# Performance work log

Measured on AMD Instinct MI355X. Metric: run time of the kernel, lower is better.

Reference implementation:

```python
import jax, jax.numpy as jnp
import numpy as np

N_LUT_IN = 4  # fan-in of every LUT node (the 'n' init arg)
KSIZE = 3


def _lut_level(x, w):
    """x: [O, N, L*n] in [0,1]; w: [O, L, 2^n] LUT tables -> [O, N, L].
    Differentiable LUT = multilinear interpolation over the 2^n corners."""
    O, L = w.shape[0], w.shape[1]
    xi = x.reshape(x.shape[0], x.shape[1], L, N_LUT_IN)
    # iterative doubling builds corner probs without a [.., 2^n, n] broadcast
    p = jnp.ones(xi.shape[:3] + (1,), xi.dtype)
    for i in range(N_LUT_IN):
        xii = xi[..., i:i + 1]
        p = jnp.concatenate([p * (1.0 - xii), p * xii], axis=-1)  # [O,N,L,2^i+1]
    return jnp.einsum('onlc,olc->onl', p, w)


def _lut_tree(flat, ws):
    """flat: [O, N, n_leaf_inputs]; ws: list of per-level LUT tables [O, L_lvl, 16]."""
    x = jax.nn.sigmoid(flat)  # squash real activations into [0,1] for interpolation
    for li, w in enumerate(ws):
        need = w.shape[1] * N_LUT_IN
        pad = need - x.shape[-1]
        if pad > 0:  # pad with 0.5 == sigmoid(0), matching zero-padding of raw inputs
            x = jnp.pad(x, ((0, 0), (0, 0), (0, pad)), constant_values=0.5)
        x = _lut_level(x, w)
        if li < len(ws) - 1:
            x = jax.nn.sigmoid(x)
    return x[..., 0]  # [O, N]


def setup_inputs() -> dict:
    key = jax.random.key(0)
    ks = jax.random.split(key, 5)
    B, C, H, W = 8, 64, 32, 32
    O, Q = 32, 8
    x = jax.random.normal(ks[0], (B, C, H, W), jnp.float32)
    rng = np.random.default_rng(0)
    ci = jnp.asarray(np.stack([rng.permutation(C)[:Q] for _ in range(O)]), jnp.int32)
    # tree level widths for 72 leaf inputs, fan-in 4: 72 -> 18 -> 5 -> 2 -> 1
    w0 = jax.random.normal(ks[1], (O, 18, 16), jnp.float32) * 0.5
    w1 = jax.random.normal(ks[2], (O, 5, 16), jnp.float32) * 0.5
    w2 = jax.random.normal(ks[3], (O, 2, 16), jnp.float32) * 0.5
    w3 = jax.random.normal(ks[4], (O, 1, 16), jnp.float32) * 0.5
    return {'x': x, 'w0': w0, 'w1': w1, 'w2': w2, 'w3': w3, 'channel_indices': ci}


def reference(x, w0, w1, w2, w3, channel_indices):
    B, C, H, W = x.shape
    K = KSIZE
    # unfold: pad=1, stride=1 -> [B, C*K*K, Ho, Wo], feature dim is channel-major (C, K, K)
    patches = jax.lax.conv_general_dilated_patches(
        x, (K, K), (1, 1), ((1, 1), (1, 1)))
    Ho, Wo = patches.shape[2], patches.shape[3]
    patches = patches.reshape(B, C, K, K, Ho, Wo)
    O, Q = channel_indices.shape
    sel = patches[:, channel_indices]  # per-out-channel gather: [B, O, Q, K, K, Ho, Wo]
    # match torch permute(0,2,3,1,4,5): leaf order per pixel is (channel, kh, kw)
    flat = sel.transpose(1, 0, 5, 6, 2, 3, 4).reshape(O, B * Ho * Wo, Q * K * K)
    out = _lut_tree(flat, [w0, w1, w2, w3])  # [O, B*Ho*Wo]
    return out.reshape(O, B, Ho, Wo).transpose(1, 0, 2, 3)  # [B, O, Ho, Wo]
```

## Files before the change

kernel.cpp:

```cpp
#include <hip/hip_runtime.h>

typedef float v2f __attribute__((ext_vector_type(2)));

#define HW 32
#define QD 8

__device__ __forceinline__ float sigmoidf(float v) {
    return __builtin_amdgcn_rcpf(1.0f + __expf(-v));
}

__device__ __forceinline__ v2f sig2(v2f v) {
    v2f r; r.x = sigmoidf(v.x); r.y = sigmoidf(v.y); return r;
}

__device__ __forceinline__ v2f lut4v(const v2f* s, const float* __restrict__ W) {
    v2f a[8];
#pragma unroll
    for (int j = 0; j < 8; ++j) {
        const float d = W[j + 8] - W[j];
        const v2f dv = {d, d}, wv = {W[j], W[j]};
        a[j] = __builtin_elementwise_fma(s[3], dv, wv);
    }
#pragma unroll
    for (int j = 0; j < 4; ++j) a[j] = __builtin_elementwise_fma(s[2], a[j + 4] - a[j], a[j]);
#pragma unroll
    for (int j = 0; j < 2; ++j) a[j] = __builtin_elementwise_fma(s[1], a[j + 2] - a[j], a[j]);
    return __builtin_elementwise_fma(s[0], a[1] - a[0], a[0]);
}

__global__ __launch_bounds__(512, 4) void lt_conv_kernel(
    const float* __restrict__ x,
    const float* __restrict__ w0,
    const float* __restrict__ w1,
    const float* __restrict__ w2,
    const float* __restrict__ w3,
    const int*   __restrict__ ci,
    float*       __restrict__ out)
{
    const int o = blockIdx.x & 31;
    const int b = blockIdx.x >> 5;
    const int tid = threadIdx.x;

    __shared__ float stile[QD * 34 * 34];
    __shared__ int   ldsci[QD];

    if (tid < QD) ldsci[tid] = ci[o * QD + tid];
    __syncthreads();

#pragma unroll
    for (int it = 0; it < 19; ++it) {
        const int idx = tid + it * 512;
        if (idx < QD * 34 * 34) {
            const int q   = idx / 1156;
            const int rem = idx - q * 1156;
            const int row = rem / 34;
            const int col = rem - row * 34;
            const int y = row - 1, xx = col - 1;
            float v = 0.0f;
            if ((unsigned)y < 32u && (unsigned)xx < 32u) {
                const int c = ldsci[q];
                v = x[(((size_t)b * 64 + c) * HW + y) * HW + xx];
            }
            stile[idx] = sigmoidf(v);
        }
    }
    __syncthreads();

    const int wo = tid & 31;
    const int r0 = (tid >> 5) * 2;

    const float* W0 = w0 + o * 18 * 16;
    v2f t[18];
#pragma unroll
    for (int l = 0; l < 18; ++l) {
        v2f p[4];
#pragma unroll
        for (int j = 0; j < 4; ++j) {
            const int flat = 4 * l + j;
            const int q = flat / 9, k = flat - 9 * q;
            const int dy = k / 3, dx = k - 3 * dy;
            const float* base = stile + q * 1156 + (r0 + dy) * 34 + (wo + dx);
            p[j].x = base[0];
            p[j].y = base[34];
        }
        t[l] = sig2(lut4v(p, W0 + l * 16));
    }

    const float* W1 = w1 + o * 5 * 16;
    const v2f h = {0.5f, 0.5f};
    v2f u[5];
#pragma unroll
    for (int l = 0; l < 4; ++l) u[l] = sig2(lut4v(t + 4 * l, W1 + l * 16));
    {
        v2f p[4] = {t[16], t[17], h, h};
        u[4] = sig2(lut4v(p, W1 + 4 * 16));
    }

    const float* W2 = w2 + o * 2 * 16;
    const v2f vv0 = sig2(lut4v(u, W2));
    v2f p1[4] = {u[4], h, h, h};
    const v2f vv1 = sig2(lut4v(p1, W2 + 16));

    const float* W3 = w3 + o * 16;
    v2f p2[4] = {vv0, vv1, h, h};
    const v2f res = lut4v(p2, W3);

    float* op = out + (((size_t)b * 32 + o) * HW + r0) * HW + wo;
    op[0]  = res.x;
    op[HW] = res.y;
}

extern "C" void kernel_launch(void* const* d_in, const int* in_sizes, int n_in,
                              void* d_out, int out_size, void* d_ws, size_t ws_size,
                              hipStream_t stream) {
    const float* x  = (const float*)d_in[0];
    const float* w0 = (const float*)d_in[1];
    const float* w1 = (const float*)d_in[2];
    const float* w2 = (const float*)d_in[3];
    const float* w3 = (const float*)d_in[4];
    const int*   ci = (const int*)d_in[5];
    float* out = (float*)d_out;

    lt_conv_kernel<<<dim3(32 * 8), dim3(512), 0, stream>>>(x, w0, w1, w2, w3, ci, out);
}
```

Before: 80.15 us.

## Split image into half-height blocks and pack two LUTs per v2f lane

Launches twice as many blocks, each covering 16 output rows with an 18-row halo tile. Each thread now computes one pixel, and the packed-float math pairs two different LUT nodes of the same level instead of two pixels. The odd nodes that do not pair up use a new scalar path. The aim is more parallelism across the GPU's CUs and lower per-thread register pressure, at the cost of extra halo loads and extra sigmoid work when filling the tile.

```diff
diff --git a/kernel.cpp b/kernel.cpp
--- a/kernel.cpp
+++ b/kernel.cpp
@@ -4,6 +4,9 @@
 
 #define HW 32
 #define QD 8
+#define ROWS 18
+#define TW 34
+#define TILE (ROWS * TW)
 
 __device__ __forceinline__ float sigmoidf(float v) {
     return __builtin_amdgcn_rcpf(1.0f + __expf(-v));
@@ -13,12 +16,13 @@
     v2f r; r.x = sigmoidf(v.x); r.y = sigmoidf(v.y); return r;
 }
 
-__device__ __forceinline__ v2f lut4v(const v2f* s, const float* __restrict__ W) {
+__device__ __forceinline__ v2f lut4p(const v2f* s, const float* __restrict__ Wa,
+                                     const float* __restrict__ Wb) {
     v2f a[8];
 #pragma unroll
     for (int j = 0; j < 8; ++j) {
-        const float d = W[j + 8] - W[j];
-        const v2f dv = {d, d}, wv = {W[j], W[j]};
+        const v2f dv = {Wa[j + 8] - Wa[j], Wb[j + 8] - Wb[j]};
+        const v2f wv = {Wa[j], Wb[j]};
         a[j] = __builtin_elementwise_fma(s[3], dv, wv);
     }
 #pragma unroll
@@ -27,6 +31,19 @@
     for (int j = 0; j < 2; ++j) a[j] = __builtin_elementwise_fma(s[1], a[j + 2] - a[j], a[j]);
     return __builtin_elementwise_fma(s[0], a[1] - a[0], a[0]);
 }
+
+__device__ __forceinline__ float lut4s(const float* s, const float* __restrict__ W) {
+    float a[8];
+#pragma unroll
+    for (int j = 0; j < 8; ++j) a[j] = fmaf(s[3], W[j + 8] - W[j], W[j]);
+#pragma unroll
+    for (int j = 0; j < 4; ++j) a[j] = fmaf(s[2], a[j + 4] - a[j], a[j]);
+#pragma unroll
+    for (int j = 0; j < 2; ++j) a[j] = fmaf(s[1], a[j + 2] - a[j], a[j]);
+    return fmaf(s[0], a[1] - a[0], a[0]);
+}
+
+#define TGET(k) (((k) & 1) ? t2[(k) >> 1].y : t2[(k) >> 1].x)
 
 __global__ __launch_bounds__(512, 4) void lt_conv_kernel(
     const float* __restrict__ x,
@@ -37,25 +54,28 @@
     const int*   __restrict__ ci,
     float*       __restrict__ out)
 {
-    const int o = blockIdx.x & 31;
-    const int b = blockIdx.x >> 5;
-    const int tid = threadIdx.x;
+    const int bi = blockIdx.x;
+    const int o = bi & 31;
+    const int b = (bi >> 5) & 7;
+    const int h = bi >> 8;
 
-    __shared__ float stile[QD * 34 * 34];
+    __shared__ float stile[QD * TILE];
     __shared__ int   ldsci[QD];
 
+    const int tid = threadIdx.x;
     if (tid < QD) ldsci[tid] = ci[o * QD + tid];
     __syncthreads();
 
+    const int y0 = h * 16 - 1;
 #pragma unroll
-    for (int it = 0; it < 19; ++it) {
+    for (int it = 0; it < 10; ++it) {
         const int idx = tid + it * 512;
-        if (idx < QD * 34 * 34) {
-            const int q   = idx / 1156;
-            const int rem = idx - q * 1156;
-            const int row = rem / 34;
-            const int col = rem - row * 34;
-            const int y = row - 1, xx = col - 1;
+        if (idx < QD * TILE) {
+            const int q   = idx / TILE;
+            const int rem = idx - q * TILE;
+            const int row = rem / TW;
+            const int col = rem - row * TW;
+            const int y = y0 + row, xx = col - 1;
             float v = 0.0f;
             if ((unsigned)y < 32u && (unsigned)xx < 32u) {
                 const int c = ldsci[q];
@@ -67,47 +87,65 @@
     __syncthreads();
 
     const int wo = tid & 31;
-    const int r0 = (tid >> 5) * 2;
+    const int r  = tid >> 5;
 
     const float* W0 = w0 + o * 18 * 16;
-    v2f t[18];
+    v2f t2[9];
 #pragma unroll
-    for (int l = 0; l < 18; ++l) {
-        v2f p[4];
+    for (int lp = 0; lp < 9; ++lp) {
+        v2f s[4];
 #pragma unroll
-        for (int j = 0; j < 4; ++j) {
-            const int flat = 4 * l + j;
-            const int q = flat / 9, k = flat - 9 * q;
-            const int dy = k / 3, dx = k - 3 * dy;
-            const float* base = stile + q * 1156 + (r0 + dy) * 34 + (wo + dx);
-            p[j].x = base[0];
-            p[j].y = base[34];
+        for (int i = 0; i < 4; ++i) {
+            {
+                const int flat = 8 * lp + i;
+                const int q = flat / 9, k = flat - 9 * q;
+                const int dy = k / 3, dx = k - 3 * dy;
+                s[i].x = stile[q * TILE + (r + dy) * TW + (wo + dx)];
+            }
+            {
+                const int flat = 8 * lp + 4 + i;
+                const int q = flat / 9, k = flat - 9 * q;
+                const int dy = k / 3, dx = k - 3 * dy;
+                s[i].y = stile[q * TILE + (r + dy) * TW + (wo + dx)];
+            }
         }
-        t[l] = sig2(lut4v(p, W0 + l * 16));
+        t2[lp] = sig2(lut4p(s, W0 + (2 * lp) * 16, W0 + (2 * lp + 1) * 16));
     }
 
     const float* W1 = w1 + o * 5 * 16;
-    const v2f h = {0.5f, 0.5f};
-    v2f u[5];
+    float u[5];
+    {
+        v2f s[4];
 #pragma unroll
-    for (int l = 0; l < 4; ++l) u[l] = sig2(lut4v(t + 4 * l, W1 + l * 16));
+        for (int i = 0; i < 4; ++i) { s[i].x = TGET(i);     s[i].y = TGET(4 + i);  }
+        const v2f r01 = sig2(lut4p(s, W1 + 0 * 16, W1 + 1 * 16));
+        u[0] = r01.x; u[1] = r01.y;
+    }
     {
-        v2f p[4] = {t[16], t[17], h, h};
-        u[4] = sig2(lut4v(p, W1 + 4 * 16));
+        v2f s[4];
+#pragma unroll
+        for (int i = 0; i < 4; ++i) { s[i].x = TGET(8 + i); s[i].y = TGET(12 + i); }
+        const v2f r23 = sig2(lut4p(s, W1 + 2 * 16, W1 + 3 * 16));
+        u[2] = r23.x; u[3] = r23.y;
+    }
+    {
+        const float s4[4] = {TGET(16), TGET(17), 0.5f, 0.5f};
+        u[4] = sigmoidf(lut4s(s4, W1 + 4 * 16));
     }
 
     const float* W2 = w2 + o * 2 * 16;
-    const v2f vv0 = sig2(lut4v(u, W2));
-    v2f p1[4] = {u[4], h, h, h};
-    const v2f vv1 = sig2(lut4v(p1, W2 + 16));
+    v2f s2v[4];
+    s2v[0].x = u[0]; s2v[0].y = u[4];
+    s2v[1].x = u[1]; s2v[1].y = 0.5f;
+    s2v[2].x = u[2]; s2v[2].y = 0.5f;
+    s2v[3].x = u[3]; s2v[3].y = 0.5f;
+    const v2f vv = sig2(lut4p(s2v, W2, W2 + 16));
 
     const float* W3 = w3 + o * 16;
-    v2f p2[4] = {vv0, vv1, h, h};
-    const v2f res = lut4v(p2, W3);
+    const float s3[4] = {vv.x, vv.y, 0.5f, 0.5f};
+    const float res = lut4s(s3, W3);
 
-    float* op = out + (((size_t)b * 32 + o) * HW + r0) * HW + wo;
-    op[0]  = res.x;
-    op[HW] = res.y;
+    out[(((size_t)b * 32 + o) * HW + (h * 16 + r)) * HW + wo] = res;
 }
 
 extern "C" void kernel_launch(void* const* d_in, const int* in_sizes, int n_in,
@@ -121,5 +159,5 @@
     const int*   ci = (const int*)d_in[5];
     float* out = (float*)d_out;
 
-    lt_conv_kernel<<<dim3(32 * 8), dim3(512), 0, stream>>>(x, w0, w1, w2, w3, ci, out);
+    lt_conv_kernel<<<dim3(32 * 8 * 2), dim3(512), 0, stream>>>(x, w0, w1, w2, w3, ci, out);
 }
```

Result: faster. 73.46 us (-8.3%).
